# Optimization experiments

Measured on AMD Instinct MI355X. Metric: run time of the kernel, lower is better.

Reference implementation:

```python
import jax, jax.numpy as jnp
import numpy as np

K = 1000      # subset size (hardcoded in SelectionHead: SubsetOperator(k=1000, hard=True))
TAU = 1.0     # gumbel-softmax temperature
EPS = float(np.finfo(np.float32).tiny)  # torch SubsetOperator uses np.finfo(np.float32).tiny


def setup_inputs() -> dict:
    key = jax.random.key(0)
    k1, k2 = jax.random.split(key)
    B, N = 4, 32768
    logits = jax.random.normal(k1, (B, N), dtype=jnp.float32)
    # gumbel noise sampled once (torch samples Gumbel(0,1) inside forward)
    gumbel = jax.random.gumbel(k2, (B, N), dtype=jnp.float32)
    return {"logits": logits, "gumbel": gumbel}


def _subset_operator(logits, gumbel):
    """Iterative Gumbel top-k relaxation (Xie & Ermon), hard straight-through."""
    scores0 = logits + gumbel                      # [B, N]
    zeros = jnp.zeros_like(scores0)

    @jax.checkpoint
    def body(carry, _):
        scores, onehot, khot = carry
        # mask out already-selected mass, renormalize via softmax
        scores = scores + jnp.log(jnp.maximum(1.0 - onehot, EPS))
        onehot = jax.nn.softmax(scores / TAU, axis=-1)
        return (scores, onehot, khot + onehot), None

    (_, _, khot), _ = jax.lax.scan(body, (scores0, zeros, zeros), None, length=K)

    # hard k-hot with straight-through estimator
    _, ind = jax.lax.top_k(khot, K)                # [B, K]
    b = khot.shape[0]
    khot_hard = zeros.at[jnp.arange(b)[:, None], ind].set(1.0)
    return khot_hard - jax.lax.stop_gradient(khot) + khot


def reference(logits, gumbel):
    values = jax.nn.sigmoid(jnp.max(logits, axis=1))          # [B]
    actions = _subset_operator(logits, gumbel)                # [B, N]
    logprobs = jax.nn.log_softmax(logits, axis=-1) * actions  # [B, N]
    return values, logprobs, actions
```

## Files before the change

### kernel.cpp

```cpp
#include <hip/hip_runtime.h>
#include <math.h>
#include <stdint.h>

#define NCOL 32768
#define NROW 4
#define KSEL 1000
#define TPB  1024
#define NW   16
#define SLC  32
#define FTH  2.0f
#define BASEU 0x40000000u
#define SHFT 14
#define BINS 1536
#define TCAP 64


__device__ __forceinline__ float wred_sum_f(float v) {
#pragma unroll
  for (int m = 32; m; m >>= 1) v += __shfl_xor(v, m, 64);
  return v;
}
__device__ __forceinline__ float wred_max_f(float v) {
#pragma unroll
  for (int m = 32; m; m >>= 1) v = fmaxf(v, __shfl_xor(v, m, 64));
  return v;
}
__device__ __forceinline__ int wsuffix_incl(int v, int lane) {
#pragma unroll
  for (int d = 1; d < 64; d <<= 1) {
    int t = __shfl_down(v, d, 64);
    if (lane + d < 64) v += t;
  }
  return v;
}
__device__ __forceinline__ uint32_t bin_of(uint32_t u) {
  uint32_t b = (u - BASEU) >> SHFT;
  return b > (BINS - 1) ? (BINS - 1) : b;
}

__global__ __launch_bounds__(TPB) void selhead_kernel(
    const float* __restrict__ logits,
    const float* __restrict__ gumbel,
    float* __restrict__ out)
{
  const int row  = blockIdx.x >> 5;
  const int slc  = blockIdx.x & 31;
  const int tid  = threadIdx.x;
  const int lane = tid & 63;
  const int wv   = tid >> 6;
  const long rowoff = (long)row * NCOL;
  const float* lrow = logits + rowoff;
  const float* grow = gumbel + rowoff;

  __shared__ uint32_t hist[BINS];
  __shared__ float    redF[NW];
  __shared__ float    redM[NW];
  __shared__ int      swtot[NW];
  __shared__ uint32_t tu[TCAP];
  __shared__ int      tc[TCAP];
  __shared__ int      tnum;
  __shared__ int      bcB, bcG;
  __shared__ uint32_t bcT;
  __shared__ int      bcC;

  for (int i = tid; i < BINS; i += TPB) hist[i] = 0;
  if (tid == 0) { tnum = 0; bcB = 0; bcG = 0; }
  __syncthreads();

  float pse = 0.f, mxl = -INFINITY;
#pragma unroll
  for (int j = 0; j < 8; ++j) {
    const int c = tid + TPB * j;
    const float4 lv = ((const float4*)lrow)[c];
    const float4 gv = ((const float4*)grow)[c];
    const float lq[4] = {lv.x, lv.y, lv.z, lv.w};
    const float gq[4] = {gv.x, gv.y, gv.z, gv.w};
#pragma unroll
    for (int q = 0; q < 4; ++q) {
      pse += __expf(lq[q]);
      mxl = fmaxf(mxl, lq[q]);
      const float s0 = lq[q] + gq[q];
      if (s0 >= FTH)
        atomicAdd(&hist[bin_of(__float_as_uint(s0))], 1u);
    }
  }
  {
    float ws = wred_sum_f(pse);
    float wm = wred_max_f(mxl);
    if (lane == 0) { redF[wv] = ws; redM[wv] = wm; }
  }
  __syncthreads();

  const int b0 = 2 * tid, b1 = 2 * tid + 1;
  const int h0 = (tid < BINS / 2) ? (int)hist[b0] : 0;
  const int h1 = (tid < BINS / 2) ? (int)hist[b1] : 0;
  const int p  = h0 + h1;
  const int sfx = wsuffix_incl(p, lane);
  if (lane == 0) swtot[wv] = sfx;
  __syncthreads();
  float SE = 0.f, ML = -INFINITY;
  int waveAbove = 0;
#pragma unroll
  for (int i = 0; i < NW; ++i) {
    SE += redF[i];
    ML = fmaxf(ML, redM[i]);
    if (i > wv) waveAbove += swtot[i];
  }
  const float logZ = logf(SE);
  if (slc == 0 && tid == 0) out[row] = 1.0f / (1.0f + expf(-ML));

  const int cbase = waveAbove + (sfx - p);
  if (cbase < KSEL && cbase + p >= KSEL) {
    const int c1 = cbase + h1;
    if (c1 >= KSEL) { bcB = b1; bcG = cbase; }
    else            { bcB = b0; bcG = c1;    }
  }
  __syncthreads();
  const int B   = bcB;
  const int cgt = bcG;

#pragma unroll
  for (int j = 0; j < 8; ++j) {
    const int c = tid + TPB * j;
    const float4 lv = ((const float4*)lrow)[c];
    const float4 gv = ((const float4*)grow)[c];
    const float lq[4] = {lv.x, lv.y, lv.z, lv.w};
    const float gq[4] = {gv.x, gv.y, gv.z, gv.w};
#pragma unroll
    for (int q = 0; q < 4; ++q) {
      const float s0 = lq[q] + gq[q];
      if (s0 >= FTH) {
        const uint32_t u = __float_as_uint(s0);
        if ((int)bin_of(u) == B) {
          const int pos = atomicAdd(&tnum, 1);
          if (pos < TCAP) { tu[pos] = u; tc[pos] = 4 * c + q; }
        }
      }
    }
  }
  __syncthreads();

  if (wv == 0) {
    int mB = tnum; if (mB > TCAP) mB = TCAP;
    const int rneed = KSEL - cgt;
    uint32_t myu = 0; int myc = 0x7FFFFFFF;
    if (lane < mB) { myu = tu[lane]; myc = tc[lane]; }
    int r = 0;
    for (int j = 0; j < mB; ++j) {
      const uint32_t uj = tu[j];
      const int cj = tc[j];
      if (uj > myu || (uj == myu && cj < myc)) ++r;
    }
    if (lane < mB && r == rneed - 1) { bcT = myu; bcC = myc; }
  }
  __syncthreads();
  const uint32_t T = bcT;
  const int idx_cut = bcC;

  {
    const int col = slc * 1024 + tid;
    const float lf = lrow[col];
    const float gf = grow[col];
    const float s0 = lf + gf;
    bool sel = false;
    if (s0 >= FTH) {
      const uint32_t u = __float_as_uint(s0);
      const uint32_t bn = bin_of(u);
      sel = (bn > (uint32_t)B) ||
            ((bn == (uint32_t)B) && (u > T || (u == T && col <= idx_cut)));
    }
    const float a = sel ? 1.0f : 0.0f;
    out[NROW + rowoff + col] = (lf - logZ) * a;
    out[NROW + (long)NROW * NCOL + rowoff + col] = a;
  }
}

extern "C" void kernel_launch(void* const* d_in, const int* in_sizes, int n_in,
                              void* d_out, int out_size, void* d_ws, size_t ws_size,
                              hipStream_t stream) {
  const float* logits = (const float*)d_in[0];
  const float* gumbel = (const float*)d_in[1];
  float* out = (float*)d_out;
  hipLaunchKernelGGL(selhead_kernel, dim3(NROW * SLC), dim3(TPB), 0, stream,
                     logits, gumbel, out);
}
```

Before: 63.07 us.

## Split row scan across workgroups with cooperative grid syncs

Before, each of the 32 workgroups per row redundantly re-read the whole 32K-element row twice to build the histogram and gather threshold candidates. Now each workgroup reads only its own 1024-element slice. Per-slice histograms and softmax partials go to a global workspace, merged after a cooperative grid sync, and threshold-bin candidates are collected globally before a second grid sync. This removes the 32x redundant global reads and ALU work, at the cost of two grid-wide barriers, a cooperative launch, and global atomics and reads of 32 histograms per row.

```diff
diff --git a/kernel.cpp b/kernel.cpp
--- a/kernel.cpp
+++ b/kernel.cpp
@@ -1,4 +1,5 @@
 #include <hip/hip_runtime.h>
+#include <hip/hip_cooperative_groups.h>
 #include <math.h>
 #include <stdint.h>
 
@@ -8,12 +9,15 @@
 #define TPB  1024
 #define NW   16
 #define SLC  32
+#define NWG  (NROW * SLC)
 #define FTH  2.0f
 #define BASEU 0x40000000u
 #define SHFT 14
 #define BINS 1536
 #define TCAP 64
 
+
+namespace cg = cooperative_groups;
 
 __device__ __forceinline__ float wred_sum_f(float v) {
 #pragma unroll
@@ -38,19 +42,27 @@
   return b > (BINS - 1) ? (BINS - 1) : b;
 }
 
-__global__ __launch_bounds__(TPB) void selhead_kernel(
+__global__ __launch_bounds__(TPB) void selhead_coop(
     const float* __restrict__ logits,
     const float* __restrict__ gumbel,
-    float* __restrict__ out)
+    float* __restrict__ out,
+    uint32_t* __restrict__ wsbuf)
 {
-  const int row  = blockIdx.x >> 5;
-  const int slc  = blockIdx.x & 31;
+  const int wg   = blockIdx.x;
+  const int row  = wg >> 5;
+  const int slc  = wg & 31;
   const int tid  = threadIdx.x;
   const int lane = tid & 63;
   const int wv   = tid >> 6;
   const long rowoff = (long)row * NCOL;
-  const float* lrow = logits + rowoff;
-  const float* grow = gumbel + rowoff;
+  const int col = (slc << 10) + tid;
+
+  uint32_t* histg = wsbuf;
+  float*    SEp   = (float*)(wsbuf + (long)NROW * SLC * BINS);
+  float*    MLp   = SEp + NROW * SLC;
+  int*      tnum  = (int*)(MLp + NROW * SLC);
+  uint32_t* twu   = (uint32_t*)(tnum + NROW);
+  int*      twc   = (int*)(twu + NROW * TCAP);
 
   __shared__ uint32_t hist[BINS];
   __shared__ float    redF[NW];
@@ -58,53 +70,64 @@
   __shared__ int      swtot[NW];
   __shared__ uint32_t tu[TCAP];
   __shared__ int      tc[TCAP];
-  __shared__ int      tnum;
   __shared__ int      bcB, bcG;
   __shared__ uint32_t bcT;
   __shared__ int      bcC;
 
   for (int i = tid; i < BINS; i += TPB) hist[i] = 0;
-  if (tid == 0) { tnum = 0; bcB = 0; bcG = 0; }
+  if (tid == 0) { bcB = 0; bcG = 0; }
   __syncthreads();
 
-  float pse = 0.f, mxl = -INFINITY;
+  const float lf = logits[rowoff + col];
+  const float gf = gumbel[rowoff + col];
+  const float s0 = lf + gf;
+  const uint32_t u = __float_as_uint(s0);
+  const bool cand = (s0 >= FTH);
+  if (cand) atomicAdd(&hist[bin_of(u)], 1u);
+  {
+    float pw = wred_sum_f(__expf(lf));
+    float mw = wred_max_f(lf);
+    if (lane == 0) { redF[wv] = pw; redM[wv] = mw; }
+  }
+  __syncthreads();
+  if (tid == 0) {
+    float se = 0.f, ml = -INFINITY;
 #pragma unroll
-  for (int j = 0; j < 8; ++j) {
-    const int c = tid + TPB * j;
-    const float4 lv = ((const float4*)lrow)[c];
-    const float4 gv = ((const float4*)grow)[c];
-    const float lq[4] = {lv.x, lv.y, lv.z, lv.w};
-    const float gq[4] = {gv.x, gv.y, gv.z, gv.w};
-#pragma unroll
-    for (int q = 0; q < 4; ++q) {
-      pse += __expf(lq[q]);
-      mxl = fmaxf(mxl, lq[q]);
-      const float s0 = lq[q] + gq[q];
-      if (s0 >= FTH)
-        atomicAdd(&hist[bin_of(__float_as_uint(s0))], 1u);
+    for (int i = 0; i < NW; ++i) { se += redF[i]; ml = fmaxf(ml, redM[i]); }
+    SEp[row * SLC + slc] = se;
+    MLp[row * SLC + slc] = ml;
+    if (slc == 0) tnum[row] = 0;
+  }
+  {
+    uint32_t* hdst = histg + ((long)row * SLC + slc) * BINS;
+    for (int i = tid; i < BINS; i += TPB) hdst[i] = hist[i];
+  }
+
+  cg::this_grid().sync();
+
+  int h0 = 0, h1 = 0;
+  if (tid < BINS / 2) {
+    const uint32_t* hrow = histg + (long)row * SLC * BINS;
+#pragma unroll 8
+    for (int w = 0; w < SLC; ++w) {
+      const uint2 hv = ((const uint2*)(hrow + w * BINS))[tid];
+      h0 += (int)hv.x;
+      h1 += (int)hv.y;
     }
   }
-  {
-    float ws = wred_sum_f(pse);
-    float wm = wred_max_f(mxl);
-    if (lane == 0) { redF[wv] = ws; redM[wv] = wm; }
-  }
-  __syncthreads();
-
-  const int b0 = 2 * tid, b1 = 2 * tid + 1;
-  const int h0 = (tid < BINS / 2) ? (int)hist[b0] : 0;
-  const int h1 = (tid < BINS / 2) ? (int)hist[b1] : 0;
-  const int p  = h0 + h1;
+  const int p   = h0 + h1;
   const int sfx = wsuffix_incl(p, lane);
   if (lane == 0) swtot[wv] = sfx;
   __syncthreads();
-  float SE = 0.f, ML = -INFINITY;
   int waveAbove = 0;
 #pragma unroll
-  for (int i = 0; i < NW; ++i) {
-    SE += redF[i];
-    ML = fmaxf(ML, redM[i]);
-    if (i > wv) waveAbove += swtot[i];
+  for (int i = 0; i < NW; ++i) if (i > wv) waveAbove += swtot[i];
+
+  float SE = 0.f, ML = -INFINITY;
+#pragma unroll 8
+  for (int w = 0; w < SLC; ++w) {
+    SE += SEp[row * SLC + w];
+    ML  = fmaxf(ML, MLp[row * SLC + w]);
   }
   const float logZ = logf(SE);
   if (slc == 0 && tid == 0) out[row] = 1.0f / (1.0f + expf(-ML));
@@ -112,36 +135,24 @@
   const int cbase = waveAbove + (sfx - p);
   if (cbase < KSEL && cbase + p >= KSEL) {
     const int c1 = cbase + h1;
-    if (c1 >= KSEL) { bcB = b1; bcG = cbase; }
-    else            { bcB = b0; bcG = c1;    }
+    if (c1 >= KSEL) { bcB = 2 * tid + 1; bcG = cbase; }
+    else            { bcB = 2 * tid;     bcG = c1;    }
   }
   __syncthreads();
   const int B   = bcB;
   const int cgt = bcG;
 
-#pragma unroll
-  for (int j = 0; j < 8; ++j) {
-    const int c = tid + TPB * j;
-    const float4 lv = ((const float4*)lrow)[c];
-    const float4 gv = ((const float4*)grow)[c];
-    const float lq[4] = {lv.x, lv.y, lv.z, lv.w};
-    const float gq[4] = {gv.x, gv.y, gv.z, gv.w};
-#pragma unroll
-    for (int q = 0; q < 4; ++q) {
-      const float s0 = lq[q] + gq[q];
-      if (s0 >= FTH) {
-        const uint32_t u = __float_as_uint(s0);
-        if ((int)bin_of(u) == B) {
-          const int pos = atomicAdd(&tnum, 1);
-          if (pos < TCAP) { tu[pos] = u; tc[pos] = 4 * c + q; }
-        }
-      }
-    }
+  if (cand && (int)bin_of(u) == B) {
+    const int pos = atomicAdd(&tnum[row], 1);
+    if (pos < TCAP) { twu[row * TCAP + pos] = u; twc[row * TCAP + pos] = col; }
   }
+
+  cg::this_grid().sync();
+
+  int mB = tnum[row]; if (mB > TCAP) mB = TCAP;
+  if (tid < mB) { tu[tid] = twu[row * TCAP + tid]; tc[tid] = twc[row * TCAP + tid]; }
   __syncthreads();
-
   if (wv == 0) {
-    int mB = tnum; if (mB > TCAP) mB = TCAP;
     const int rneed = KSEL - cgt;
     uint32_t myu = 0; int myc = 0x7FFFFFFF;
     if (lane < mB) { myu = tu[lane]; myc = tc[lane]; }
@@ -157,22 +168,15 @@
   const uint32_t T = bcT;
   const int idx_cut = bcC;
 
-  {
-    const int col = slc * 1024 + tid;
-    const float lf = lrow[col];
-    const float gf = grow[col];
-    const float s0 = lf + gf;
-    bool sel = false;
-    if (s0 >= FTH) {
-      const uint32_t u = __float_as_uint(s0);
-      const uint32_t bn = bin_of(u);
-      sel = (bn > (uint32_t)B) ||
-            ((bn == (uint32_t)B) && (u > T || (u == T && col <= idx_cut)));
-    }
-    const float a = sel ? 1.0f : 0.0f;
-    out[NROW + rowoff + col] = (lf - logZ) * a;
-    out[NROW + (long)NROW * NCOL + rowoff + col] = a;
+  bool sel = false;
+  if (cand) {
+    const uint32_t bn = bin_of(u);
+    sel = (bn > (uint32_t)B) ||
+          ((bn == (uint32_t)B) && (u > T || (u == T && col <= idx_cut)));
   }
+  const float a = sel ? 1.0f : 0.0f;
+  out[NROW + rowoff + col] = (lf - logZ) * a;
+  out[NROW + (long)NROW * NCOL + rowoff + col] = a;
 }
 
 extern "C" void kernel_launch(void* const* d_in, const int* in_sizes, int n_in,
@@ -181,6 +185,8 @@
   const float* logits = (const float*)d_in[0];
   const float* gumbel = (const float*)d_in[1];
   float* out = (float*)d_out;
-  hipLaunchKernelGGL(selhead_kernel, dim3(NROW * SLC), dim3(TPB), 0, stream,
-                     logits, gumbel, out);
+  uint32_t* wsbuf = (uint32_t*)d_ws;
+  void* args[] = { (void*)&logits, (void*)&gumbel, (void*)&out, (void*)&wsbuf };
+  hipLaunchCooperativeKernel((const void*)selhead_coop, dim3(NWG), dim3(TPB),
+                             args, 0, stream);
 }
```

After: 107.9 us. 71.1% more time.
